# Kernel tuning notes

Hardware: AMD Instinct MI355X
Metric: run time of the kernel (lower is better)

The kernel has to match this reference:

```python
import jax, jax.numpy as jnp
import numpy as np

F_DIM = 128
H_DIM = 64
N_NODES = 100000
N_EDGES = 1000000
BN_EPS = 1e-5

def setup_inputs() -> dict:
    key = jax.random.key(0)
    ks = jax.random.split(key, 10)
    x = jax.random.normal(ks[0], (N_NODES, F_DIM), dtype=jnp.float32)
    edges = jax.random.randint(ks[1], (2, N_EDGES), 0, N_NODES, dtype=jnp.int64)
    s_in = 1.0 / np.sqrt(2 * F_DIM)
    s_h = 1.0 / np.sqrt(H_DIM)
    W_in = jax.random.uniform(ks[2], (H_DIM, 2 * F_DIM), jnp.float32, -s_in, s_in)
    b_in = jax.random.uniform(ks[3], (H_DIM,), jnp.float32, -s_in, s_in)
    W_h = jax.random.uniform(ks[4], (H_DIM, H_DIM), jnp.float32, -s_h, s_h)
    b_h = jax.random.uniform(ks[5], (H_DIM,), jnp.float32, -s_h, s_h)
    gamma = jnp.ones((H_DIM,), jnp.float32)
    beta = jnp.zeros((H_DIM,), jnp.float32)
    W_out = jax.random.uniform(ks[6], (1, H_DIM), jnp.float32, -s_h, s_h)
    b_out = jax.random.uniform(ks[7], (1,), jnp.float32, -s_h, s_h)
    return {"x": x, "edges": edges, "W_in": W_in, "b_in": b_in,
            "W_h": W_h, "b_h": b_h, "gamma": gamma, "beta": beta,
            "W_out": W_out, "b_out": b_out}

def reference(x, edges, W_in, b_in, W_h, b_h, gamma, beta, W_out, b_out):
    # gather node pair features and concat -> [E, 2F]
    ef = jnp.concatenate((x[edges[0]], x[edges[1]]), axis=1)
    h = jax.nn.relu(ef @ W_in.T + b_in)          # [E, H]
    h = h @ W_h.T + b_h                           # hidden linear
    # BatchNorm1d in training mode: batch stats over edge dim (biased var)
    mean = jnp.mean(h, axis=0)
    var = jnp.mean((h - mean) ** 2, axis=0)
    h = (h - mean) * jax.lax.rsqrt(var + BN_EPS) * gamma + beta
    h = jax.nn.relu(h)
    edge_scores = (h @ W_out.T + b_out).squeeze(-1)  # [E]
    return edge_scores
```

## Files before the change

kernel.cpp:

```cpp
#include <hip/hip_runtime.h>
#include <hip/hip_bf16.h>
#include <hip/hip_fp16.h>

#define N_NODES 100000
#define N_EDGES 1000000
#define BN_EPS 1e-5f
#define N_CHUNKS (N_EDGES / 64)

typedef __attribute__((ext_vector_type(8))) short bf16x8;
typedef __attribute__((ext_vector_type(4))) float f32x4;


__device__ __forceinline__ unsigned pk2(float a, float b) {
  unsigned ua = __builtin_bit_cast(unsigned, a);
  unsigned ub = __builtin_bit_cast(unsigned, b);
  ua += 0x7fffu + ((ua >> 16) & 1u);
  ub += 0x7fffu + ((ub >> 16) & 1u);
  return (ua >> 16) | (ub & 0xffff0000u);
}

__device__ __forceinline__ bf16x8 pack8(float4 v0, float4 v1) {
  uint4 u = make_uint4(pk2(v0.x, v0.y), pk2(v0.z, v0.w), pk2(v1.x, v1.y), pk2(v1.z, v1.w));
  return __builtin_bit_cast(bf16x8, u);
}

__device__ __forceinline__ bf16x8 frag_relu_add(uint4 a, uint4 d) {
  uint4 r;
  const unsigned* aw = (const unsigned*)&a;
  const unsigned* dw = (const unsigned*)&d;
  unsigned* rw = (unsigned*)&r;
#pragma unroll
  for (int q = 0; q < 4; ++q) {
    const float alo = __builtin_bit_cast(float, aw[q] << 16);
    const float ahi = __builtin_bit_cast(float, aw[q] & 0xffff0000u);
    const float dlo = __builtin_bit_cast(float, dw[q] << 16);
    const float dhi = __builtin_bit_cast(float, dw[q] & 0xffff0000u);
    rw[q] = pk2(fmaxf(alo + dlo, 0.f), fmaxf(ahi + dhi, 0.f));
  }
  return __builtin_bit_cast(bf16x8, r);
}

__device__ __forceinline__ void load_bfr(const float* __restrict__ W_h, int l15, int l4,
                                         bf16x8 bfr[4][2]) {
#pragma unroll
  for (int nt = 0; nt < 4; ++nt)
#pragma unroll
    for (int kk = 0; kk < 2; ++kk) {
      const float* wp = W_h + (16 * nt + l15) * 64 + (kk * 4 + l4) * 8;
      bfr[nt][kk] = pack8(*(const float4*)wp, *(const float4*)(wp + 4));
    }
}

__global__ __launch_bounds__(64) void k_probe(const unsigned* __restrict__ eu,
                                              int* __restrict__ flag) {
  if (threadIdx.x == 0) {
    unsigned acc = 0;
#pragma unroll
    for (int i = 1; i < 64; i += 2) acc |= eu[i];
    *flag = (acc == 0) ? 1 : 0;
  }
}

__global__ __launch_bounds__(256) void k1_mfma(
    const float* __restrict__ x, const float* __restrict__ W_in,
    const float* __restrict__ b_in, __hip_bfloat16* __restrict__ A,
    float* __restrict__ stats) {
  const int t = threadIdx.x;
  if (blockIdx.x == 0 && t < 128) stats[t] = 0.f;
  const int lane = t & 63;
  const int w = t >> 6;
  const int l15 = lane & 15, l4 = lane >> 4;
  const int nb = blockIdx.x * 128 + (w >> 1) * 64;
  const int cb = (w & 1) * 64;

  bf16x8 wfrag[4][4];
#pragma unroll
  for (int ct = 0; ct < 4; ++ct) {
#pragma unroll
    for (int kk = 0; kk < 4; ++kk) {
      const float* wp = W_in + (16 * ct + l15) * 256 + (cb ? 128 : 0) + 32 * kk + 8 * l4;
      wfrag[ct][kk] = pack8(*(const float4*)wp, *(const float4*)(wp + 4));
    }
  }
  f32x4 acc[4][4];
#pragma unroll
  for (int nt = 0; nt < 4; ++nt)
#pragma unroll
    for (int ct = 0; ct < 4; ++ct)
      acc[nt][ct] = (f32x4){0.f, 0.f, 0.f, 0.f};

#pragma unroll
  for (int nt = 0; nt < 4; ++nt) {
    int node = nb + 16 * nt + l15;
    node = node < N_NODES ? node : N_NODES - 1;
    const float* xr = x + (size_t)node * 128 + 8 * l4;
#pragma unroll
    for (int kk = 0; kk < 4; ++kk) {
      const bf16x8 xf = pack8(*(const float4*)(xr + 32 * kk), *(const float4*)(xr + 32 * kk + 4));
#pragma unroll
      for (int ct = 0; ct < 4; ++ct)
        acc[nt][ct] = __builtin_amdgcn_mfma_f32_16x16x32_bf16(wfrag[ct][kk], xf, acc[nt][ct], 0, 0, 0);
    }
  }

  float4 bv[4];
#pragma unroll
  for (int ct = 0; ct < 4; ++ct)
    bv[ct] = cb ? make_float4(0.f, 0.f, 0.f, 0.f) : *(const float4*)(b_in + 16 * ct + 4 * l4);
#pragma unroll
  for (int nt = 0; nt < 4; ++nt) {
    const int node = nb + 16 * nt + l15;
    if (node < N_NODES) {
      __hip_bfloat16* ap = A + (size_t)node * 128 + cb + 4 * l4;
#pragma unroll
      for (int ct = 0; ct < 4; ++ct) {
        uint2 u;
        u.x = pk2(acc[nt][ct][0] + bv[ct].x, acc[nt][ct][1] + bv[ct].y);
        u.y = pk2(acc[nt][ct][2] + bv[ct].z, acc[nt][ct][3] + bv[ct].w);
        *(uint2*)(ap + 16 * ct) = u;
      }
    }
  }
}

template<bool STORE_G>
__global__ __launch_bounds__(256) void k2_stats(
    const __hip_bfloat16* __restrict__ A, const void* __restrict__ edges,
    const int* __restrict__ flag, const float* __restrict__ W_h,
    float* __restrict__ stats, __half* __restrict__ g) {
  const int lane = threadIdx.x & 63;
  const int l15 = lane & 15, l4 = lane >> 4;
  bf16x8 bfr[4][2];
  load_bfr(W_h, l15, l4, bfr);

  const int is64 = *flag;
  const long long* e64 = (const long long*)edges;
  const int* e32 = (const int*)edges;
  float vs[4] = {0.f, 0.f, 0.f, 0.f};
  float vq[4] = {0.f, 0.f, 0.f, 0.f};
  const int gwave = blockIdx.x * 4 + (threadIdx.x >> 6);
  const int nwaves = gridDim.x * 4;
  for (int chunk = gwave; chunk < N_CHUNKS; chunk += nwaves) {
    const int base = chunk * 64;
#pragma unroll
    for (int mt = 0; mt < 4; ++mt) {
      const int eidx = base + mt * 16 + l15;
      int s, d;
      if (is64) { s = (int)e64[eidx]; d = (int)e64[N_EDGES + eidx]; }
      else      { s = e32[eidx];      d = e32[N_EDGES + eidx]; }
      const uint4* As = (const uint4*)(A + (size_t)s * 128);
      const uint4* Ad = (const uint4*)(A + (size_t)d * 128 + 64);
      const uint4 as0 = As[l4], as1 = As[4 + l4];
      const uint4 ad0 = Ad[l4], ad1 = Ad[4 + l4];
      const bf16x8 a0 = frag_relu_add(as0, ad0);
      const bf16x8 a1 = frag_relu_add(as1, ad1);
#pragma unroll
      for (int nt = 0; nt < 4; ++nt) {
        f32x4 c = {0.f, 0.f, 0.f, 0.f};
        c = __builtin_amdgcn_mfma_f32_16x16x32_bf16(a0, bfr[nt][0], c, 0, 0, 0);
        c = __builtin_amdgcn_mfma_f32_16x16x32_bf16(a1, bfr[nt][1], c, 0, 0, 0);
        if (STORE_G) {
          const __half2 h0 = __floats2half2_rn(c[0], c[1]);
          const __half2 h1 = __floats2half2_rn(c[2], c[3]);
          uint2 u;
          u.x = __builtin_bit_cast(unsigned, h0);
          u.y = __builtin_bit_cast(unsigned, h1);
          *(uint2*)(g + ((((size_t)chunk * 4 + mt) * 4 + nt) * 64 + lane) * 4) = u;
        }
#pragma unroll
        for (int j = 0; j < 4; ++j) {
          vs[nt] += c[j];
          vq[nt] += c[j] * c[j];
        }
      }
    }
  }
#pragma unroll
  for (int nt = 0; nt < 4; ++nt) {
    float s1 = vs[nt], s2 = vq[nt];
    s1 += __shfl_xor(s1, 16, 64); s1 += __shfl_xor(s1, 32, 64);
    s2 += __shfl_xor(s2, 16, 64); s2 += __shfl_xor(s2, 32, 64);
    if (lane < 16) {
      atomicAdd(&stats[lane + 16 * nt], s1);
      atomicAdd(&stats[64 + lane + 16 * nt], s2);
    }
  }
}

__global__ __launch_bounds__(64) void k3_finalize(
    const float* __restrict__ stats, const float* __restrict__ gamma,
    const float* __restrict__ beta, float* __restrict__ ss) {
  const int c = threadIdx.x;
  if (c < 64) {
    const float inv_e = 1.f / (float)N_EDGES;
    const float mg = stats[c] * inv_e;
    const float var = stats[64 + c] * inv_e - mg * mg;
    const float scale = gamma[c] * rsqrtf(var + BN_EPS);
    ss[c] = scale;
    ss[64 + c] = beta[c] - scale * mg;
  }
}

__global__ __launch_bounds__(256) void k4_stream(
    const __half* __restrict__ g, const float* __restrict__ ss,
    const float* __restrict__ W_out, const float* __restrict__ b_out,
    float* __restrict__ out) {
  const int lane = threadIdx.x & 63;
  const int l15 = lane & 15, l4 = lane >> 4;
  float scl[4], shf[4], wo[4];
#pragma unroll
  for (int nt = 0; nt < 4; ++nt) {
    scl[nt] = ss[l15 + 16 * nt];
    shf[nt] = ss[64 + l15 + 16 * nt];
    wo[nt] = W_out[l15 + 16 * nt];
  }
  const float bo = b_out[0];
  const int gwave = blockIdx.x * 4 + (threadIdx.x >> 6);
  const int nwaves = gridDim.x * 4;
  for (int chunk = gwave; chunk < N_CHUNKS; chunk += nwaves) {
#pragma unroll
    for (int mt = 0; mt < 4; ++mt) {
      float t0 = 0.f, t1 = 0.f, t2 = 0.f, t3 = 0.f;
#pragma unroll
      for (int nt = 0; nt < 4; ++nt) {
        const uint2 u = *(const uint2*)(g + ((((size_t)chunk * 4 + mt) * 4 + nt) * 64 + lane) * 4);
        const __half2 h0 = __builtin_bit_cast(__half2, u.x);
        const __half2 h1 = __builtin_bit_cast(__half2, u.y);
        t0 += fmaxf(fmaf(__low2float(h0),  scl[nt], shf[nt]), 0.f) * wo[nt];
        t1 += fmaxf(fmaf(__high2float(h0), scl[nt], shf[nt]), 0.f) * wo[nt];
        t2 += fmaxf(fmaf(__low2float(h1),  scl[nt], shf[nt]), 0.f) * wo[nt];
        t3 += fmaxf(fmaf(__high2float(h1), scl[nt], shf[nt]), 0.f) * wo[nt];
      }
      const int ebase = chunk * 64 + mt * 16 + 4 * l4;
#pragma unroll
      for (int j = 0; j < 4; ++j) {
        float r = (j == 0) ? t0 : (j == 1) ? t1 : (j == 2) ? t2 : t3;
        r += __shfl_xor(r, 1, 64);
        r += __shfl_xor(r, 2, 64);
        r += __shfl_xor(r, 4, 64);
        r += __shfl_xor(r, 8, 64);
        if (l15 == 0) out[ebase + j] = r + bo;
      }
    }
  }
}

__global__ __launch_bounds__(256) void k4_gather(
    const __hip_bfloat16* __restrict__ A, const void* __restrict__ edges,
    const int* __restrict__ flag, const float* __restrict__ W_h,
    const float* __restrict__ ss, const float* __restrict__ W_out,
    const float* __restrict__ b_out, float* __restrict__ out) {
  const int lane = threadIdx.x & 63;
  const int l15 = lane & 15, l4 = lane >> 4;
  bf16x8 bfr[4][2];
  load_bfr(W_h, l15, l4, bfr);
  float scl[4], shf[4], wo[4];
#pragma unroll
  for (int nt = 0; nt < 4; ++nt) {
    scl[nt] = ss[l15 + 16 * nt];
    shf[nt] = ss[64 + l15 + 16 * nt];
    wo[nt] = W_out[l15 + 16 * nt];
  }
  const float bo = b_out[0];
  const int is64 = *flag;
  const long long* e64 = (const long long*)edges;
  const int* e32 = (const int*)edges;
  const int gwave = blockIdx.x * 4 + (threadIdx.x >> 6);
  const int nwaves = gridDim.x * 4;
  for (int chunk = gwave; chunk < N_CHUNKS; chunk += nwaves) {
    const int base = chunk * 64;
#pragma unroll
    for (int mt = 0; mt < 4; ++mt) {
      const int eidx = base + mt * 16 + l15;
      int s, d;
      if (is64) { s = (int)e64[eidx]; d = (int)e64[N_EDGES + eidx]; }
      else      { s = e32[eidx];      d = e32[N_EDGES + eidx]; }
      const uint4* As = (const uint4*)(A + (size_t)s * 128);
      const uint4* Ad = (const uint4*)(A + (size_t)d * 128 + 64);
      const bf16x8 a0 = frag_relu_add(As[l4], Ad[l4]);
      const bf16x8 a1 = frag_relu_add(As[4 + l4], Ad[4 + l4]);
      float t0 = 0.f, t1 = 0.f, t2 = 0.f, t3 = 0.f;
#pragma unroll
      for (int nt = 0; nt < 4; ++nt) {
        f32x4 c = {0.f, 0.f, 0.f, 0.f};
        c = __builtin_amdgcn_mfma_f32_16x16x32_bf16(a0, bfr[nt][0], c, 0, 0, 0);
        c = __builtin_amdgcn_mfma_f32_16x16x32_bf16(a1, bfr[nt][1], c, 0, 0, 0);
        t0 += fmaxf(fmaf(c[0], scl[nt], shf[nt]), 0.f) * wo[nt];
        t1 += fmaxf(fmaf(c[1], scl[nt], shf[nt]), 0.f) * wo[nt];
        t2 += fmaxf(fmaf(c[2], scl[nt], shf[nt]), 0.f) * wo[nt];
        t3 += fmaxf(fmaf(c[3], scl[nt], shf[nt]), 0.f) * wo[nt];
      }
      const int ebase = base + mt * 16 + 4 * l4;
#pragma unroll
      for (int j = 0; j < 4; ++j) {
        float r = (j == 0) ? t0 : (j == 1) ? t1 : (j == 2) ? t2 : t3;
        r += __shfl_xor(r, 1, 64);
        r += __shfl_xor(r, 2, 64);
        r += __shfl_xor(r, 4, 64);
        r += __shfl_xor(r, 8, 64);
        if (l15 == 0) out[ebase + j] = r + bo;
      }
    }
  }
}

extern "C" void kernel_launch(void* const* d_in, const int* in_sizes, int n_in,
                              void* d_out, int out_size, void* d_ws, size_t ws_size,
                              hipStream_t stream) {
  const float* x     = (const float*)d_in[0];
  const void*  edges = d_in[1];
  const float* W_in  = (const float*)d_in[2];
  const float* b_in  = (const float*)d_in[3];
  const float* W_h   = (const float*)d_in[4];
  const float* gamma = (const float*)d_in[6];
  const float* beta  = (const float*)d_in[7];
  const float* W_out = (const float*)d_in[8];
  const float* b_out = (const float*)d_in[9];
  float* out = (float*)d_out;

  char* base = (char*)d_ws;
  __hip_bfloat16* A = (__hip_bfloat16*)base;
  const size_t offStats = (size_t)N_NODES * 128 * sizeof(__hip_bfloat16);
  float* stats = (float*)(base + offStats);
  float* ss    = stats + 128;
  int*   flag  = (int*)(ss + 128);
  const size_t offG = offStats + 4096;
  __half* g = (__half*)(base + offG);
  const bool use_g = ws_size >= offG + (size_t)N_EDGES * 64 * sizeof(__half);

  k_probe<<<1, 64, 0, stream>>>((const unsigned*)edges, flag);
  k1_mfma<<<782, 256, 0, stream>>>(x, W_in, b_in, A, stats);
  if (use_g) {
    k2_stats<true><<<1024, 256, 0, stream>>>(A, edges, flag, W_h, stats, g);
    k3_finalize<<<1, 64, 0, stream>>>(stats, gamma, beta, ss);
    k4_stream<<<1024, 256, 0, stream>>>(g, ss, W_out, b_out, out);
  } else {
    k2_stats<false><<<1024, 256, 0, stream>>>(A, edges, flag, W_h, stats, g);
    k3_finalize<<<1, 64, 0, stream>>>(stats, gamma, beta, ss);
    k4_gather<<<1024, 256, 0, stream>>>(A, edges, flag, W_h, ss, W_out, b_out, out);
  }
}
```

Before: 219.9 us.

## Bucket edges by source node range to localize gathers in stats pass

Adds histogram, scan and scatter kernels that partition edges into 8 buckets by source node index. Each block group of the stats kernel then processes one bucket, so the source-row gathers of A stay within a smaller node range for better cache locality. The output kernel writes scores back through the saved edge permutation. This adds three extra passes over the edge list, a scattered output write and extra workspace, and only runs when the workspace is large enough.

```diff
diff --git a/kernel.cpp b/kernel.cpp
--- a/kernel.cpp
+++ b/kernel.cpp
@@ -6,6 +6,7 @@
 #define N_EDGES 1000000
 #define BN_EPS 1e-5f
 #define N_CHUNKS (N_EDGES / 64)
+#define NODES_PER_BUCKET 12500
 
 typedef __attribute__((ext_vector_type(8))) short bf16x8;
 typedef __attribute__((ext_vector_type(4))) float f32x4;
@@ -51,6 +52,13 @@
     }
 }
 
+__device__ __forceinline__ bool probe_is64(const void* edges) {
+  const unsigned* eu = (const unsigned*)edges;
+  const int lane = threadIdx.x & 63;
+  unsigned pw = (lane < 32) ? eu[2 * lane + 1] : 0u;
+  return __ballot(pw != 0) == 0;
+}
+
 __global__ __launch_bounds__(64) void k_probe(const unsigned* __restrict__ eu,
                                               int* __restrict__ flag) {
   if (threadIdx.x == 0) {
@@ -58,6 +66,100 @@
 #pragma unroll
     for (int i = 1; i < 64; i += 2) acc |= eu[i];
     *flag = (acc == 0) ? 1 : 0;
+  }
+}
+
+__global__ __launch_bounds__(256) void k_hist(const void* __restrict__ edges,
+                                              unsigned* __restrict__ partial) {
+  const int t = threadIdx.x, lane = t & 63, wid = t >> 6;
+  const bool is64 = probe_is64(edges);
+  const long long* e64 = (const long long*)edges;
+  const int* e32 = (const int*)edges;
+  unsigned mycnt = 0;
+  for (int e = blockIdx.x * 256 + t; e < N_EDGES; e += gridDim.x * 256) {
+    const int s = is64 ? (int)e64[e] : e32[e];
+    const unsigned b = (unsigned)s / NODES_PER_BUCKET;
+#pragma unroll
+    for (int b8 = 0; b8 < 8; ++b8) {
+      const unsigned long long m = __ballot(b == (unsigned)b8);
+      if (lane == b8) mycnt += (unsigned)__popcll(m);
+    }
+  }
+  if (lane < 8) partial[(blockIdx.x * 4 + wid) * 8 + lane] = mycnt;
+}
+
+__global__ __launch_bounds__(64) void k_scan(const unsigned* __restrict__ partial,
+                                             unsigned* __restrict__ cursor,
+                                             int* __restrict__ cb) {
+  __shared__ unsigned red[8][8];
+  const int t = threadIdx.x;
+  const int b = t & 7, gidx = t >> 3;
+  unsigned s = 0;
+  for (int i = gidx; i < 2048; i += 8) s += partial[i * 8 + b];
+  red[gidx][b] = s;
+  __syncthreads();
+  if (t < 8) {
+    unsigned tot = 0;
+#pragma unroll
+    for (int g2 = 0; g2 < 8; ++g2) tot += red[g2][t];
+    red[0][t] = tot;
+  }
+  __syncthreads();
+  if (t == 0) {
+    unsigned run = 0;
+    cb[0] = 0;
+    for (int b2 = 0; b2 < 8; ++b2) {
+      cursor[b2] = run;
+      run += red[0][b2];
+      cb[b2 + 1] = (b2 == 7) ? N_CHUNKS : (int)(run >> 6);
+    }
+  }
+}
+
+__global__ __launch_bounds__(256) void k_scatter(const void* __restrict__ edges,
+                                                 unsigned* __restrict__ cursor,
+                                                 int* __restrict__ sp,
+                                                 int* __restrict__ dp,
+                                                 int* __restrict__ eord) {
+  __shared__ unsigned wcnt[4][8];
+  __shared__ unsigned woff[4][8];
+  __shared__ unsigned bbase[8];
+  const int t = threadIdx.x, lane = t & 63, wid = t >> 6;
+  const bool is64 = probe_is64(edges);
+  const long long* e64 = (const long long*)edges;
+  const int* e32 = (const int*)edges;
+  const int stride = gridDim.x * 256;
+  const int niter = (N_EDGES + stride - 1) / stride;
+  int e = blockIdx.x * 256 + t;
+  for (int it = 0; it < niter; ++it, e += stride) {
+    const bool valid = e < N_EDGES;
+    int s = 0, d = 0;
+    if (valid) {
+      if (is64) { s = (int)e64[e]; d = (int)e64[N_EDGES + e]; }
+      else      { s = e32[e];      d = e32[N_EDGES + e]; }
+    }
+    const unsigned b = (unsigned)s / NODES_PER_BUCKET;
+    unsigned long long mymask = 0;
+#pragma unroll
+    for (int b8 = 0; b8 < 8; ++b8) {
+      const unsigned long long m = __ballot(valid && (b == (unsigned)b8));
+      if (valid && b == (unsigned)b8) mymask = m;
+      if (lane == b8) wcnt[wid][b8] = (unsigned)__popcll(m);
+    }
+    __syncthreads();
+    if (t < 8) {
+      const unsigned c0 = wcnt[0][t], c1 = wcnt[1][t], c2 = wcnt[2][t], c3 = wcnt[3][t];
+      woff[0][t] = 0; woff[1][t] = c0; woff[2][t] = c0 + c1; woff[3][t] = c0 + c1 + c2;
+      const unsigned tot = c0 + c1 + c2 + c3;
+      bbase[t] = tot ? atomicAdd(&cursor[t], tot) : 0u;
+    }
+    __syncthreads();
+    if (valid) {
+      const unsigned pos = bbase[b] + woff[wid][b] +
+                           (unsigned)__popcll(mymask & ((1ull << lane) - 1ull));
+      sp[pos] = s; dp[pos] = d; eord[pos] = e;
+    }
+    __syncthreads();
   }
 }
 
@@ -123,6 +225,129 @@
   }
 }
 
+__global__ __launch_bounds__(256) void k2p_stats(
+    const __hip_bfloat16* __restrict__ A, const int* __restrict__ sp,
+    const int* __restrict__ dp, const int* __restrict__ cb,
+    const float* __restrict__ W_h, float* __restrict__ stats,
+    __half* __restrict__ g) {
+  const int lane = threadIdx.x & 63;
+  const int wid = threadIdx.x >> 6;
+  const int l15 = lane & 15, l4 = lane >> 4;
+  bf16x8 bfr[4][2];
+  load_bfr(W_h, l15, l4, bfr);
+
+  const int xb = blockIdx.x & 7;
+  const int c0 = cb[xb], c1 = cb[xb + 1];
+  const int wstride = (gridDim.x >> 3) * 4;
+  float vs[4] = {0.f, 0.f, 0.f, 0.f};
+  float vq[4] = {0.f, 0.f, 0.f, 0.f};
+  for (int c = c0 + (blockIdx.x >> 3) * 4 + wid; c < c1; c += wstride) {
+    const int sA = sp[c * 64 + lane];
+    const int dA = dp[c * 64 + lane];
+#pragma unroll
+    for (int mt = 0; mt < 4; ++mt) {
+      const int s = __shfl(sA, mt * 16 + l15, 64);
+      const int d = __shfl(dA, mt * 16 + l15, 64);
+      const uint4* As = (const uint4*)(A + (size_t)s * 128);
+      const uint4* Ad = (const uint4*)(A + (size_t)d * 128 + 64);
+      const bf16x8 a0 = frag_relu_add(As[l4], Ad[l4]);
+      const bf16x8 a1 = frag_relu_add(As[4 + l4], Ad[4 + l4]);
+#pragma unroll
+      for (int nt = 0; nt < 4; ++nt) {
+        f32x4 cacc = {0.f, 0.f, 0.f, 0.f};
+        cacc = __builtin_amdgcn_mfma_f32_16x16x32_bf16(a0, bfr[nt][0], cacc, 0, 0, 0);
+        cacc = __builtin_amdgcn_mfma_f32_16x16x32_bf16(a1, bfr[nt][1], cacc, 0, 0, 0);
+        const __half2 h0 = __floats2half2_rn(cacc[0], cacc[1]);
+        const __half2 h1 = __floats2half2_rn(cacc[2], cacc[3]);
+        uint2 u;
+        u.x = __builtin_bit_cast(unsigned, h0);
+        u.y = __builtin_bit_cast(unsigned, h1);
+        *(uint2*)(g + ((((size_t)c * 4 + mt) * 4 + nt) * 64 + lane) * 4) = u;
+#pragma unroll
+        for (int j = 0; j < 4; ++j) {
+          vs[nt] += cacc[j];
+          vq[nt] += cacc[j] * cacc[j];
+        }
+      }
+    }
+  }
+#pragma unroll
+  for (int nt = 0; nt < 4; ++nt) {
+    float s1 = vs[nt], s2 = vq[nt];
+    s1 += __shfl_xor(s1, 16, 64); s1 += __shfl_xor(s1, 32, 64);
+    s2 += __shfl_xor(s2, 16, 64); s2 += __shfl_xor(s2, 32, 64);
+    if (lane < 16) {
+      atomicAdd(&stats[lane + 16 * nt], s1);
+      atomicAdd(&stats[64 + lane + 16 * nt], s2);
+    }
+  }
+}
+
+__global__ __launch_bounds__(64) void k3_finalize(
+    const float* __restrict__ stats, const float* __restrict__ gamma,
+    const float* __restrict__ beta, float* __restrict__ ss) {
+  const int c = threadIdx.x;
+  if (c < 64) {
+    const float inv_e = 1.f / (float)N_EDGES;
+    const float mg = stats[c] * inv_e;
+    const float var = stats[64 + c] * inv_e - mg * mg;
+    const float scale = gamma[c] * rsqrtf(var + BN_EPS);
+    ss[c] = scale;
+    ss[64 + c] = beta[c] - scale * mg;
+  }
+}
+
+__global__ __launch_bounds__(256) void k4p_out(
+    const __half* __restrict__ g, const int* __restrict__ eord,
+    const float* __restrict__ ss, const float* __restrict__ W_out,
+    const float* __restrict__ b_out, float* __restrict__ out) {
+  const int lane = threadIdx.x & 63;
+  const int l15 = lane & 15, l4 = lane >> 4;
+  float scl[4], shf[4], wo[4];
+#pragma unroll
+  for (int nt = 0; nt < 4; ++nt) {
+    scl[nt] = ss[l15 + 16 * nt];
+    shf[nt] = ss[64 + l15 + 16 * nt];
+    wo[nt] = W_out[l15 + 16 * nt];
+  }
+  const float bo = b_out[0];
+  const int gwave = blockIdx.x * 4 + (threadIdx.x >> 6);
+  const int nwaves = gridDim.x * 4;
+  for (int chunk = gwave; chunk < N_CHUNKS; chunk += nwaves) {
+#pragma unroll
+    for (int mt = 0; mt < 4; ++mt) {
+      float t0 = 0.f, t1 = 0.f, t2 = 0.f, t3 = 0.f;
+#pragma unroll
+      for (int nt = 0; nt < 4; ++nt) {
+        const uint2 u = *(const uint2*)(g + ((((size_t)chunk * 4 + mt) * 4 + nt) * 64 + lane) * 4);
+        const __half2 h0 = __builtin_bit_cast(__half2, u.x);
+        const __half2 h1 = __builtin_bit_cast(__half2, u.y);
+        t0 += fmaxf(fmaf(__low2float(h0),  scl[nt], shf[nt]), 0.f) * wo[nt];
+        t1 += fmaxf(fmaf(__high2float(h0), scl[nt], shf[nt]), 0.f) * wo[nt];
+        t2 += fmaxf(fmaf(__low2float(h1),  scl[nt], shf[nt]), 0.f) * wo[nt];
+        t3 += fmaxf(fmaf(__high2float(h1), scl[nt], shf[nt]), 0.f) * wo[nt];
+      }
+      float rr[4];
+#pragma unroll
+      for (int j = 0; j < 4; ++j) {
+        float r = (j == 0) ? t0 : (j == 1) ? t1 : (j == 2) ? t2 : t3;
+        r += __shfl_xor(r, 1, 64);
+        r += __shfl_xor(r, 2, 64);
+        r += __shfl_xor(r, 4, 64);
+        r += __shfl_xor(r, 8, 64);
+        rr[j] = r + bo;
+      }
+      if (l15 == 0) {
+        const uint4 eq = *(const uint4*)(eord + chunk * 64 + mt * 16 + 4 * l4);
+        out[(int)eq.x] = rr[0];
+        out[(int)eq.y] = rr[1];
+        out[(int)eq.z] = rr[2];
+        out[(int)eq.w] = rr[3];
+      }
+    }
+  }
+}
+
 template<bool STORE_G>
 __global__ __launch_bounds__(256) void k2_stats(
     const __hip_bfloat16* __restrict__ A, const void* __restrict__ edges,
@@ -132,7 +357,6 @@
   const int l15 = lane & 15, l4 = lane >> 4;
   bf16x8 bfr[4][2];
   load_bfr(W_h, l15, l4, bfr);
-
   const int is64 = *flag;
   const long long* e64 = (const long long*)edges;
   const int* e32 = (const int*)edges;
@@ -150,10 +374,8 @@
       else      { s = e32[eidx];      d = e32[N_EDGES + eidx]; }
       const uint4* As = (const uint4*)(A + (size_t)s * 128);
       const uint4* Ad = (const uint4*)(A + (size_t)d * 128 + 64);
-      const uint4 as0 = As[l4], as1 = As[4 + l4];
-      const uint4 ad0 = Ad[l4], ad1 = Ad[4 + l4];
-      const bf16x8 a0 = frag_relu_add(as0, ad0);
-      const bf16x8 a1 = frag_relu_add(as1, ad1);
+      const bf16x8 a0 = frag_relu_add(As[l4], Ad[l4]);
+      const bf16x8 a1 = frag_relu_add(As[4 + l4], Ad[4 + l4]);
 #pragma unroll
       for (int nt = 0; nt < 4; ++nt) {
         f32x4 c = {0.f, 0.f, 0.f, 0.f};
@@ -184,20 +406,6 @@
       atomicAdd(&stats[lane + 16 * nt], s1);
       atomicAdd(&stats[64 + lane + 16 * nt], s2);
     }
-  }
-}
-
-__global__ __launch_bounds__(64) void k3_finalize(
-    const float* __restrict__ stats, const float* __restrict__ gamma,
-    const float* __restrict__ beta, float* __restrict__ ss) {
-  const int c = threadIdx.x;
-  if (c < 64) {
-    const float inv_e = 1.f / (float)N_EDGES;
-    const float mg = stats[c] * inv_e;
-    const float var = stats[64 + c] * inv_e - mg * mg;
-    const float scale = gamma[c] * rsqrtf(var + BN_EPS);
-    ss[c] = scale;
-    ss[64 + c] = beta[c] - scale * mg;
   }
 }
 
@@ -320,22 +528,42 @@
 
   char* base = (char*)d_ws;
   __hip_bfloat16* A = (__hip_bfloat16*)base;
-  const size_t offStats = (size_t)N_NODES * 128 * sizeof(__hip_bfloat16);
-  float* stats = (float*)(base + offStats);
-  float* ss    = stats + 128;
-  int*   flag  = (int*)(ss + 128);
-  const size_t offG = offStats + 4096;
-  __half* g = (__half*)(base + offG);
-  const bool use_g = ws_size >= offG + (size_t)N_EDGES * 64 * sizeof(__half);
-
-  k_probe<<<1, 64, 0, stream>>>((const unsigned*)edges, flag);
-  k1_mfma<<<782, 256, 0, stream>>>(x, W_in, b_in, A, stats);
-  if (use_g) {
-    k2_stats<true><<<1024, 256, 0, stream>>>(A, edges, flag, W_h, stats, g);
+  const size_t offMeta = (size_t)N_NODES * 128 * sizeof(__hip_bfloat16);
+  float*    stats   = (float*)(base + offMeta);
+  float*    ss      = stats + 128;
+  int*      flag    = (int*)(base + offMeta + 1024);
+  unsigned* cursor  = (unsigned*)(base + offMeta + 1088);
+  int*      cbArr   = (int*)(base + offMeta + 1120);
+  unsigned* partial = (unsigned*)(base + offMeta + 4096);
+  const size_t offSp = offMeta + 4096 + 65536;
+  int* sp   = (int*)(base + offSp);
+  int* dp   = sp + N_EDGES;
+  int* eord = dp + N_EDGES;
+  __half* gS = (__half*)(base + offSp + 3 * (size_t)N_EDGES * 4);
+  const size_t needSorted = offSp + 3 * (size_t)N_EDGES * 4 + (size_t)N_EDGES * 64 * 2;
+
+  __half* gF = (__half*)(base + offMeta + 4096);
+  const bool sorted = ws_size >= needSorted;
+  const bool use_g  = ws_size >= offMeta + 4096 + (size_t)N_EDGES * 64 * 2;
+
+  if (sorted) {
+    k_hist<<<512, 256, 0, stream>>>(edges, partial);
+    k_scan<<<1, 64, 0, stream>>>(partial, cursor, cbArr);
+    k_scatter<<<512, 256, 0, stream>>>(edges, cursor, sp, dp, eord);
+    k1_mfma<<<782, 256, 0, stream>>>(x, W_in, b_in, A, stats);
+    k2p_stats<<<2048, 256, 0, stream>>>(A, sp, dp, cbArr, W_h, stats, gS);
     k3_finalize<<<1, 64, 0, stream>>>(stats, gamma, beta, ss);
-    k4_stream<<<1024, 256, 0, stream>>>(g, ss, W_out, b_out, out);
+    k4p_out<<<2048, 256, 0, stream>>>(gS, eord, ss, W_out, b_out, out);
+  } else if (use_g) {
+    k_probe<<<1, 64, 0, stream>>>((const unsigned*)edges, flag);
+    k1_mfma<<<782, 256, 0, stream>>>(x, W_in, b_in, A, stats);
+    k2_stats<true><<<1024, 256, 0, stream>>>(A, edges, flag, W_h, stats, gF);
+    k3_finalize<<<1, 64, 0, stream>>>(stats, gamma, beta, ss);
+    k4_stream<<<1024, 256, 0, stream>>>(gF, ss, W_out, b_out, out);
   } else {
-    k2_stats<false><<<1024, 256, 0, stream>>>(A, edges, flag, W_h, stats, g);
+    k_probe<<<1, 64, 0, stream>>>((const unsigned*)edges, flag);
+    k1_mfma<<<782, 256, 0, stream>>>(x, W_in, b_in, A, stats);
+    k2_stats<false><<<1024, 256, 0, stream>>>(A, edges, flag, W_h, stats, gF);
     k3_finalize<<<1, 64, 0, stream>>>(stats, gamma, beta, ss);
     k4_gather<<<1024, 256, 0, stream>>>(A, edges, flag, W_h, ss, W_out, b_out, out);
   }
```

Measured after the change: 383.2 us. +74.2%, slower.
